# Performance work log

Hardware: AMD Instinct MI355X
Metric: run time of the kernel (lower is better)

Reference implementation:

```python
import jax, jax.numpy as jnp
import numpy as np

N = 50000        # nodes
E = 1_600_000    # edges (avg degree 32)
IN, HID, OUT = 128, 64, 16


def setup_inputs() -> dict:
    key = jax.random.key(0)
    k0, k1, k2, k3, k4 = jax.random.split(key, 5)
    src = jax.random.randint(k0, (E,), 0, N, dtype=jnp.int32)
    dst = jax.random.randint(k1, (E,), 0, N, dtype=jnp.int32)
    features = jax.random.normal(k2, (N, IN), dtype=jnp.float32)
    W1 = jax.random.normal(k3, (IN, HID), dtype=jnp.float32) / np.float32(np.sqrt(IN))
    b1 = jnp.zeros((HID,), jnp.float32)
    W2 = jax.random.normal(k4, (HID, OUT), dtype=jnp.float32) / np.float32(np.sqrt(HID))
    b2 = jnp.zeros((OUT,), jnp.float32)
    return {"features": features, "W1": W1, "b1": b1, "W2": W2, "b2": b2,
            "src": src, "dst": dst}


def _graph_conv(src, dst, x, W, b):
    # DGL GraphConv, norm='both':  out = D_dst^{-1/2} * A^T * (D_src^{-1/2} * x) @ W + b
    ones = jnp.ones((src.shape[0],), x.dtype)
    deg_out = jax.ops.segment_sum(ones, src, num_segments=N)  # out-degree of source nodes
    deg_in = jax.ops.segment_sum(ones, dst, num_segments=N)   # in-degree of dest nodes
    norm_s = jax.lax.rsqrt(jnp.maximum(deg_out, 1.0))
    norm_d = jax.lax.rsqrt(jnp.maximum(deg_in, 1.0))
    # project first (in_feats >= out_feats) so messages are in the smaller dim
    h = (x * norm_s[:, None]) @ W                              # [N, out_dim]
    agg = jax.ops.segment_sum(h[src], dst, num_segments=N)     # sparse aggregate
    return agg * norm_d[:, None] + b


def reference(features, W1, b1, W2, b2, src, dst):
    h = jax.nn.relu(_graph_conv(src, dst, features, W1, b1))
    return _graph_conv(src, dst, h, W2, b2)
```

## Files before the change

kernel.cpp:

```cpp
#include <hip/hip_runtime.h>
#include <hip/hip_fp16.h>

#define IN_F  128
#define HID_F 64
#define OUT_F 16
#define MAX_N 50176
#define HWORDS (MAX_N / 2)
#define QWORDS (MAX_N / 4)
#define NSEG  128

#define SCAN_ELEMS 4
#define SCAN_BLOCK 256
#define SCAN_CHUNK (SCAN_BLOCK * SCAN_ELEMS)

#define LSTR 136

typedef __attribute__((ext_vector_type(8))) _Float16 half8;
typedef __attribute__((ext_vector_type(4))) _Float16 half4v;
typedef __attribute__((ext_vector_type(4))) float    floatx4;

__global__ __launch_bounds__(1024) void hist2_kernel(const int* __restrict__ src,
                                                     const int* __restrict__ dst,
                                                     unsigned int* __restrict__ partial,
                                                     int E, int seg, int Wr8) {
    __shared__ unsigned int cnt[QWORDS];
    int b = blockIdx.x;
    const int* ids = blockIdx.y ? dst : src;
    unsigned int* pbase = partial + (size_t)blockIdx.y * NSEG * Wr8;
    for (int w = threadIdx.x; w < Wr8; w += 1024) cnt[w] = 0;
    __syncthreads();
    int lo = b * seg, hi = min(lo + seg, E);
    for (int e = lo + threadIdx.x; e < hi; e += 1024) {
        int d = ids[e];
        atomicAdd(&cnt[d >> 2], 1u << ((d & 3) * 8));
    }
    __syncthreads();
    for (int w = threadIdx.x; w < Wr8; w += 1024)
        pbase[(size_t)b * Wr8 + w] = cnt[w];
}

__global__ __launch_bounds__(256) void reduce_norm_kernel(unsigned int* __restrict__ partial,
                                                          int* __restrict__ counts,
                                                          float* __restrict__ norm_s,
                                                          float* __restrict__ norm_d,
                                                          int Wr8, int N) {
    int w = blockIdx.x * 256 + threadIdx.x;
    if (w >= Wr8) return;
    unsigned int r0 = 0, r1 = 0, r2 = 0, r3 = 0;
    if (blockIdx.y == 0) {
        const unsigned int* base = partial;
        for (int b = 0; b < NSEG; b++) {
            unsigned int v = base[(size_t)b * Wr8 + w];
            r0 += v & 0xFFu; r1 += (v >> 8) & 0xFFu;
            r2 += (v >> 16) & 0xFFu; r3 += v >> 24;
        }
        int d = 4 * w;
        if (d     < N) norm_s[d]     = rsqrtf(fmaxf((float)r0, 1.0f));
        if (d + 1 < N) norm_s[d + 1] = rsqrtf(fmaxf((float)r1, 1.0f));
        if (d + 2 < N) norm_s[d + 2] = rsqrtf(fmaxf((float)r2, 1.0f));
        if (d + 3 < N) norm_s[d + 3] = rsqrtf(fmaxf((float)r3, 1.0f));
    } else {
        unsigned int* base = partial + (size_t)NSEG * Wr8;
        for (int b = 0; b < NSEG; b++) {
            size_t idx = (size_t)b * Wr8 + w;
            unsigned int v = base[idx];
            base[idx] = r0 | (r1 << 8) | (r2 << 16) | (r3 << 24);
            r0 += v & 0xFFu; r1 += (v >> 8) & 0xFFu;
            r2 += (v >> 16) & 0xFFu; r3 += v >> 24;
        }
        int d = 4 * w;
        if (d     < N) { counts[d]     = (int)r0; norm_d[d]     = rsqrtf(fmaxf((float)r0, 1.0f)); }
        if (d + 1 < N) { counts[d + 1] = (int)r1; norm_d[d + 1] = rsqrtf(fmaxf((float)r1, 1.0f)); }
        if (d + 2 < N) { counts[d + 2] = (int)r2; norm_d[d + 2] = rsqrtf(fmaxf((float)r2, 1.0f)); }
        if (d + 3 < N) { counts[d + 3] = (int)r3; norm_d[d + 3] = rsqrtf(fmaxf((float)r3, 1.0f)); }
    }
}

__global__ __launch_bounds__(SCAN_BLOCK) void scan_local_kernel(int* __restrict__ counts,
                                                                int* __restrict__ bsum, int N) {
    __shared__ int part[SCAN_BLOCK];
    int t = threadIdx.x;
    int base = blockIdx.x * SCAN_CHUNK + t * SCAN_ELEMS;
    int v[SCAN_ELEMS];
    int s = 0;
    #pragma unroll
    for (int k = 0; k < SCAN_ELEMS; k++) {
        int i = base + k;
        v[k] = (i < N) ? counts[i] : 0;
        s += v[k];
    }
    part[t] = s;
    __syncthreads();
    for (int off = 1; off < SCAN_BLOCK; off <<= 1) {
        int x = (t >= off) ? part[t - off] : 0;
        __syncthreads();
        part[t] += x;
        __syncthreads();
    }
    int run = (t > 0) ? part[t - 1] : 0;
    #pragma unroll
    for (int k = 0; k < SCAN_ELEMS; k++) {
        int i = base + k;
        if (i < N) counts[i] = run;
        run += v[k];
    }
    if (t == SCAN_BLOCK - 1) bsum[blockIdx.x] = part[SCAN_BLOCK - 1];
}

__global__ __launch_bounds__(1024) void scan_bsum_kernel(int* __restrict__ bsum, int nblocks) {
    __shared__ int part[1024];
    int t = threadIdx.x;
    int v = (t < nblocks) ? bsum[t] : 0;
    part[t] = v;
    __syncthreads();
    for (int off = 1; off < 1024; off <<= 1) {
        int x = (t >= off) ? part[t - off] : 0;
        __syncthreads();
        part[t] += x;
        __syncthreads();
    }
    if (t < nblocks) bsum[t] = part[t] - v;
}

__global__ __launch_bounds__(1024) void scatter_lds_kernel(const int* __restrict__ src,
                                                           const int* __restrict__ dst,
                                                           const int* __restrict__ row_start,
                                                           const int* __restrict__ bsum,
                                                           const unsigned int* __restrict__ prefix,
                                                           unsigned short* __restrict__ csr_src,
                                                           int E, int seg, int Wr8, int N) {
    __shared__ unsigned int pos[HWORDS];
    int b = blockIdx.x;
    int p = blockIdx.y;
    int lo = b * seg, hi = min(lo + seg, E);
    int nlo = p * HWORDS, nhi = min(nlo + HWORDS, N);
    for (int d = nlo + threadIdx.x; d < nhi; d += 1024) {
        unsigned int word = prefix[(size_t)b * Wr8 + (d >> 2)];
        unsigned int base8 = (word >> ((d & 3) * 8)) & 0xFFu;
        pos[d - nlo] = (unsigned int)(row_start[d] + bsum[d >> 10]) + base8;
    }
    __syncthreads();
    for (int e = lo + threadIdx.x; e < hi; e += 1024) {
        int d = dst[e];
        if (d >= nlo && d < nhi) {
            unsigned int q = atomicAdd(&pos[d - nlo], 1u);
            csr_src[q] = (unsigned short)src[e];
        }
    }
}

__global__ __launch_bounds__(256) void gemm1_kernel(const float* __restrict__ x,
                                                    const float* __restrict__ W,
                                                    const float* __restrict__ norm_s,
                                                    __half* __restrict__ h, int N) {
    __shared__ _Float16 sx[64 * LSTR];
    __shared__ _Float16 sw[64 * LSTR];
    int t = threadIdx.x;
    int row0 = blockIdx.x * 64;

    for (int i = t; i < IN_F * 16; i += 256) {
        int k = i >> 4, n4 = (i & 15) * 4;
        float4 w4 = *(const float4*)(W + (size_t)k * HID_F + n4);
        sw[(n4 + 0) * LSTR + k] = (_Float16)w4.x;
        sw[(n4 + 1) * LSTR + k] = (_Float16)w4.y;
        sw[(n4 + 2) * LSTR + k] = (_Float16)w4.z;
        sw[(n4 + 3) * LSTR + k] = (_Float16)w4.w;
    }
    for (int i = t; i < 64 * 32; i += 256) {
        int r = i >> 5, k4 = (i & 31) * 4;
        int gr = row0 + r;
        half4v hv = {0, 0, 0, 0};
        if (gr < N) {
            float4 v = *(const float4*)(x + (size_t)gr * IN_F + k4);
            float ns = norm_s[gr];
            hv.x = (_Float16)(v.x * ns); hv.y = (_Float16)(v.y * ns);
            hv.z = (_Float16)(v.z * ns); hv.w = (_Float16)(v.w * ns);
        }
        *(half4v*)(sx + r * LSTR + k4) = hv;
    }
    __syncthreads();

    int wave = t >> 6, lane = t & 63;
    int m = lane & 15, quad = lane >> 4;
    int rbase = wave * 16;

    floatx4 acc[4] = {{0,0,0,0}, {0,0,0,0}, {0,0,0,0}, {0,0,0,0}};
    #pragma unroll
    for (int ks = 0; ks < 4; ks++) {
        half8 av = *(half8*)(sx + (rbase + m) * LSTR + ks * 32 + quad * 8);
        #pragma unroll
        for (int ct = 0; ct < 4; ct++) {
            half8 bv = *(half8*)(sw + (ct * 16 + m) * LSTR + ks * 32 + quad * 8);
            acc[ct] = __builtin_amdgcn_mfma_f32_16x16x32_f16(av, bv, acc[ct], 0, 0, 0);
        }
    }
    #pragma unroll
    for (int ct = 0; ct < 4; ct++) {
        #pragma unroll
        for (int reg = 0; reg < 4; reg++) {
            int gr = row0 + rbase + quad * 4 + reg;
            if (gr < N) h[(size_t)gr * HID_F + ct * 16 + m] = __float2half(acc[ct][reg]);
        }
    }
}

__global__ __launch_bounds__(256) void agg1_kernel(const int* __restrict__ row_start,
                                                   const int* __restrict__ bsum,
                                                   const unsigned short* __restrict__ csr_src,
                                                   const __half* __restrict__ h,
                                                   const float* __restrict__ norm_d,
                                                   const float* __restrict__ norm_s,
                                                   const float* __restrict__ b1,
                                                   const float* __restrict__ W2,
                                                   __half* __restrict__ h2, int N, int E) {
    __shared__ float sW2[HID_F * OUT_F];
    __shared__ float xrow[4][HID_F];
    int t = threadIdx.x;
    for (int i = t; i < HID_F * OUT_F; i += 256) sW2[i] = W2[i];

    int wave = t >> 6, lane = t & 63;
    int node = blockIdx.x * 4 + wave;
    bool valid = node < N;
    int slot = lane >> 3;
    int fh   = lane & 7;

    if (valid) {
        int beg = row_start[node] + bsum[node >> 10];
        int end = (node + 1 < N) ? row_start[node + 1] + bsum[(node + 1) >> 10] : E;

        float f[8] = {0.f, 0.f, 0.f, 0.f, 0.f, 0.f, 0.f, 0.f};

        #define AGG1_BODY(SIDX) {                                                  \
            const uint4* p = (const uint4*)(h + (size_t)(SIDX) * HID_F + fh * 8);  \
            uint4 u = *p;                                                          \
            __half2 q0 = *(__half2*)&u.x, q1 = *(__half2*)&u.y;                    \
            __half2 q2 = *(__half2*)&u.z, q3 = *(__half2*)&u.w;                    \
            float2 g0 = __half22float2(q0), g1 = __half22float2(q1);               \
            float2 g2 = __half22float2(q2), g3 = __half22float2(q3);               \
            f[0] += g0.x; f[1] += g0.y; f[2] += g1.x; f[3] += g1.y;                \
            f[4] += g2.x; f[5] += g2.y; f[6] += g3.x; f[7] += g3.y; }

        int i = beg + slot;
        for (; i + 24 < end; i += 32) {
            int s0 = (int)csr_src[i];
            int s1 = (int)csr_src[i + 8];
            int s2 = (int)csr_src[i + 16];
            int s3 = (int)csr_src[i + 24];
            AGG1_BODY(s0); AGG1_BODY(s1); AGG1_BODY(s2); AGG1_BODY(s3);
        }
        for (; i < end; i += 8) {
            int s = (int)csr_src[i];
            AGG1_BODY(s);
        }
        #undef AGG1_BODY

        #pragma unroll
        for (int j = 0; j < 8; j++) {
            f[j] += __shfl_xor(f[j], 8);
            f[j] += __shfl_xor(f[j], 16);
            f[j] += __shfl_xor(f[j], 32);
        }

        if (slot == 0) {
            float nd = norm_d[node], ns = norm_s[node];
            const float4 bA = *(const float4*)(b1 + fh * 8);
            const float4 bB = *(const float4*)(b1 + fh * 8 + 4);
            xrow[wave][fh * 8 + 0] = fmaxf(f[0] * nd + bA.x, 0.f) * ns;
            xrow[wave][fh * 8 + 1] = fmaxf(f[1] * nd + bA.y, 0.f) * ns;
            xrow[wave][fh * 8 + 2] = fmaxf(f[2] * nd + bA.z, 0.f) * ns;
            xrow[wave][fh * 8 + 3] = fmaxf(f[3] * nd + bA.w, 0.f) * ns;
            xrow[wave][fh * 8 + 4] = fmaxf(f[4] * nd + bB.x, 0.f) * ns;
            xrow[wave][fh * 8 + 5] = fmaxf(f[5] * nd + bB.y, 0.f) * ns;
            xrow[wave][fh * 8 + 6] = fmaxf(f[6] * nd + bB.z, 0.f) * ns;
            xrow[wave][fh * 8 + 7] = fmaxf(f[7] * nd + bB.w, 0.f) * ns;
        }
    }
    __syncthreads();
    if (valid && lane < OUT_F) {
        float acc = 0.0f;
        #pragma unroll 8
        for (int k = 0; k < HID_F; k++)
            acc += xrow[wave][k] * sW2[k * OUT_F + lane];
        h2[(size_t)node * OUT_F + lane] = __float2half(acc);
    }
}

__global__ __launch_bounds__(256) void agg2_kernel(const int* __restrict__ row_start,
                                                   const int* __restrict__ bsum,
                                                   const unsigned short* __restrict__ csr_src,
                                                   const __half* __restrict__ h2,
                                                   const float* __restrict__ norm_d,
                                                   const float* __restrict__ b2,
                                                   float* __restrict__ out, int N, int E) {
    int node = blockIdx.x * 4 + (threadIdx.x >> 6);
    if (node >= N) return;
    int lane = threadIdx.x & 63;
    int slot = lane >> 2;
    int fh   = lane & 3;
    int beg = row_start[node] + bsum[node >> 10];
    int end = (node + 1 < N) ? row_start[node + 1] + bsum[(node + 1) >> 10] : E;

    float f0 = 0.f, f1 = 0.f, f2 = 0.f, f3 = 0.f;

    #define AGG2_BODY(SIDX) {                                                  \
        const uint2* p = (const uint2*)(h2 + (size_t)(SIDX) * OUT_F + fh * 4); \
        uint2 u = *p;                                                          \
        __half2 q0 = *(__half2*)&u.x, q1 = *(__half2*)&u.y;                    \
        float2 g0 = __half22float2(q0), g1 = __half22float2(q1);               \
        f0 += g0.x; f1 += g0.y; f2 += g1.x; f3 += g1.y; }

    int i = beg + slot;
    for (; i + 16 < end; i += 32) {
        int s0 = (int)csr_src[i];
        int s1 = (int)csr_src[i + 16];
        AGG2_BODY(s0); AGG2_BODY(s1);
    }
    if (i < end) {
        int s = (int)csr_src[i];
        AGG2_BODY(s);
    }
    #undef AGG2_BODY

    f0 += __shfl_xor(f0, 4);  f1 += __shfl_xor(f1, 4);
    f2 += __shfl_xor(f2, 4);  f3 += __shfl_xor(f3, 4);
    f0 += __shfl_xor(f0, 8);  f1 += __shfl_xor(f1, 8);
    f2 += __shfl_xor(f2, 8);  f3 += __shfl_xor(f3, 8);
    f0 += __shfl_xor(f0, 16); f1 += __shfl_xor(f1, 16);
    f2 += __shfl_xor(f2, 16); f3 += __shfl_xor(f3, 16);
    f0 += __shfl_xor(f0, 32); f1 += __shfl_xor(f1, 32);
    f2 += __shfl_xor(f2, 32); f3 += __shfl_xor(f3, 32);

    if (slot == 0) {
        float nd = norm_d[node];
        float4 v;
        v.x = f0 * nd + b2[fh * 4 + 0];
        v.y = f1 * nd + b2[fh * 4 + 1];
        v.z = f2 * nd + b2[fh * 4 + 2];
        v.w = f3 * nd + b2[fh * 4 + 3];
        *(float4*)(out + (size_t)node * OUT_F + fh * 4) = v;
    }
}

extern "C" void kernel_launch(void* const* d_in, const int* in_sizes, int n_in,
                              void* d_out, int out_size, void* d_ws, size_t ws_size,
                              hipStream_t stream) {
    const float* feat = (const float*)d_in[0];
    const float* W1   = (const float*)d_in[1];
    const float* b1   = (const float*)d_in[2];
    const float* W2   = (const float*)d_in[3];
    const float* b2   = (const float*)d_in[4];
    const int*   src  = (const int*)d_in[5];
    const int*   dst  = (const int*)d_in[6];

    const int N   = in_sizes[0] / IN_F;
    const int E   = in_sizes[5];
    const int seg = (E + NSEG - 1) / NSEG;
    const int Wr8 = (N + 3) >> 2;
    const int nchunks = (N + SCAN_CHUNK - 1) / SCAN_CHUNK;
    const int npass   = (N + HWORDS - 1) / HWORDS;

    float* fws    = (float*)d_ws;
    float* norm_s = fws;
    float* norm_d = fws + N;
    __half* h1    = (__half*)(fws + 2 * (size_t)N);
    __half* h2    = h1 + (size_t)N * HID_F;
    int*   iws    = (int*)(h2 + (size_t)N * OUT_F);
    int*   row_start = iws;
    int*   bsum      = iws + N + 1;
    unsigned int* partial = (unsigned int*)(iws + N + 1 + 1024);
    unsigned short* csr_src = (unsigned short*)(partial + 2 * (size_t)NSEG * Wr8);

    hist2_kernel<<<dim3(NSEG, 2), 1024, 0, stream>>>(src, dst, partial, E, seg, Wr8);
    reduce_norm_kernel<<<dim3((Wr8 + 255) / 256, 2), 256, 0, stream>>>(partial, row_start, norm_s, norm_d, Wr8, N);

    scan_local_kernel<<<nchunks, SCAN_BLOCK, 0, stream>>>(row_start, bsum, N);
    scan_bsum_kernel<<<1, 1024, 0, stream>>>(bsum, nchunks);

    scatter_lds_kernel<<<dim3(NSEG, npass), 1024, 0, stream>>>(src, dst, row_start, bsum,
                                                               partial + (size_t)NSEG * Wr8,
                                                               csr_src, E, seg, Wr8, N);

    gemm1_kernel<<<(N + 63) / 64, 256, 0, stream>>>(feat, W1, norm_s, h1, N);
    agg1_kernel<<<(N + 3) / 4, 256, 0, stream>>>(row_start, bsum, csr_src, h1, norm_d, norm_s, b1, W2, h2, N, E);
    agg2_kernel<<<(N + 3) / 4, 256, 0, stream>>>(row_start, bsum, csr_src, h2, norm_d, b2, (float*)d_out, N, E);
}
```

Measured before the change: 212.5 us.

## Process 16 nodes per block in agg1 and use all threads for W2 projection

Each wave in agg1 now aggregates four consecutive nodes instead of one. Row-start offsets are loaded once per wave, and the W2 staging in shared memory is amortised over 16 nodes per block instead of 4. The 64x16 projection now runs across all 256 threads using a transposed, padded W2 and float4 shared-memory reads, where previously only 16 lanes per wave did the work. The cost is less block-level parallelism (about 3.1k blocks) and serial per-node latency within each wave, which may reduce how well gather latency is hidden.

```diff
diff --git a/kernel.cpp b/kernel.cpp
--- a/kernel.cpp
+++ b/kernel.cpp
@@ -14,6 +14,7 @@
 #define SCAN_CHUNK (SCAN_BLOCK * SCAN_ELEMS)
 
 #define LSTR 136
+#define XSTR 68
 
 typedef __attribute__((ext_vector_type(8))) _Float16 half8;
 typedef __attribute__((ext_vector_type(4))) _Float16 half4v;
@@ -213,75 +214,96 @@
                                                    const float* __restrict__ b1,
                                                    const float* __restrict__ W2,
                                                    __half* __restrict__ h2, int N, int E) {
-    __shared__ float sW2[HID_F * OUT_F];
-    __shared__ float xrow[4][HID_F];
+    __shared__ float sW2T[OUT_F][XSTR];
+    __shared__ float xrow[16][XSTR];
     int t = threadIdx.x;
-    for (int i = t; i < HID_F * OUT_F; i += 256) sW2[i] = W2[i];
+    for (int i = t; i < HID_F * OUT_F; i += 256) {
+        int k = i >> 4, o = i & 15;
+        sW2T[o][k] = W2[i];
+    }
 
     int wave = t >> 6, lane = t & 63;
-    int node = blockIdx.x * 4 + wave;
-    bool valid = node < N;
     int slot = lane >> 3;
     int fh   = lane & 7;
-
-    if (valid) {
-        int beg = row_start[node] + bsum[node >> 10];
-        int end = (node + 1 < N) ? row_start[node + 1] + bsum[(node + 1) >> 10] : E;
-
-        float f[8] = {0.f, 0.f, 0.f, 0.f, 0.f, 0.f, 0.f, 0.f};
-
-        #define AGG1_BODY(SIDX) {                                                  \
-            const uint4* p = (const uint4*)(h + (size_t)(SIDX) * HID_F + fh * 8);  \
-            uint4 u = *p;                                                          \
-            __half2 q0 = *(__half2*)&u.x, q1 = *(__half2*)&u.y;                    \
-            __half2 q2 = *(__half2*)&u.z, q3 = *(__half2*)&u.w;                    \
-            float2 g0 = __half22float2(q0), g1 = __half22float2(q1);               \
-            float2 g2 = __half22float2(q2), g3 = __half22float2(q3);               \
-            f[0] += g0.x; f[1] += g0.y; f[2] += g1.x; f[3] += g1.y;                \
-            f[4] += g2.x; f[5] += g2.y; f[6] += g3.x; f[7] += g3.y; }
-
-        int i = beg + slot;
-        for (; i + 24 < end; i += 32) {
-            int s0 = (int)csr_src[i];
-            int s1 = (int)csr_src[i + 8];
-            int s2 = (int)csr_src[i + 16];
-            int s3 = (int)csr_src[i + 24];
-            AGG1_BODY(s0); AGG1_BODY(s1); AGG1_BODY(s2); AGG1_BODY(s3);
-        }
-        for (; i < end; i += 8) {
-            int s = (int)csr_src[i];
-            AGG1_BODY(s);
-        }
-        #undef AGG1_BODY
-
+    int nbase = blockIdx.x * 16 + wave * 4;
+
+    int rs[5];
+    #pragma unroll
+    for (int j = 0; j < 5; j++) {
+        int n = nbase + j;
+        rs[j] = (n < N) ? (row_start[n] + bsum[n >> 10]) : E;
+    }
+
+    #pragma unroll
+    for (int nn = 0; nn < 4; nn++) {
+        int node = nbase + nn;
+        if (node < N) {
+            int beg = rs[nn], end = rs[nn + 1];
+
+            float f[8] = {0.f, 0.f, 0.f, 0.f, 0.f, 0.f, 0.f, 0.f};
+
+            #define AGG1_BODY(SIDX) {                                                  \
+                const uint4* p = (const uint4*)(h + (size_t)(SIDX) * HID_F + fh * 8);  \
+                uint4 u = *p;                                                          \
+                __half2 q0 = *(__half2*)&u.x, q1 = *(__half2*)&u.y;                    \
+                __half2 q2 = *(__half2*)&u.z, q3 = *(__half2*)&u.w;                    \
+                float2 g0 = __half22float2(q0), g1 = __half22float2(q1);               \
+                float2 g2 = __half22float2(q2), g3 = __half22float2(q3);               \
+                f[0] += g0.x; f[1] += g0.y; f[2] += g1.x; f[3] += g1.y;                \
+                f[4] += g2.x; f[5] += g2.y; f[6] += g3.x; f[7] += g3.y; }
+
+            int i = beg + slot;
+            for (; i + 24 < end; i += 32) {
+                int s0 = (int)csr_src[i];
+                int s1 = (int)csr_src[i + 8];
+                int s2 = (int)csr_src[i + 16];
+                int s3 = (int)csr_src[i + 24];
+                AGG1_BODY(s0); AGG1_BODY(s1); AGG1_BODY(s2); AGG1_BODY(s3);
+            }
+            for (; i < end; i += 8) {
+                int s = (int)csr_src[i];
+                AGG1_BODY(s);
+            }
+            #undef AGG1_BODY
+
+            #pragma unroll
+            for (int j = 0; j < 8; j++) {
+                f[j] += __shfl_xor(f[j], 8);
+                f[j] += __shfl_xor(f[j], 16);
+                f[j] += __shfl_xor(f[j], 32);
+            }
+
+            if (slot == 0) {
+                float nd = norm_d[node], ns = norm_s[node];
+                const float4 bA = *(const float4*)(b1 + fh * 8);
+                const float4 bB = *(const float4*)(b1 + fh * 8 + 4);
+                float4 vA, vB;
+                vA.x = fmaxf(f[0] * nd + bA.x, 0.f) * ns;
+                vA.y = fmaxf(f[1] * nd + bA.y, 0.f) * ns;
+                vA.z = fmaxf(f[2] * nd + bA.z, 0.f) * ns;
+                vA.w = fmaxf(f[3] * nd + bA.w, 0.f) * ns;
+                vB.x = fmaxf(f[4] * nd + bB.x, 0.f) * ns;
+                vB.y = fmaxf(f[5] * nd + bB.y, 0.f) * ns;
+                vB.z = fmaxf(f[6] * nd + bB.z, 0.f) * ns;
+                vB.w = fmaxf(f[7] * nd + bB.w, 0.f) * ns;
+                *(float4*)&xrow[wave * 4 + nn][fh * 8]     = vA;
+                *(float4*)&xrow[wave * 4 + nn][fh * 8 + 4] = vB;
+            }
+        }
+    }
+    __syncthreads();
+
+    int nr = t >> 4, o = t & 15;
+    int gnode = blockIdx.x * 16 + nr;
+    if (gnode < N) {
+        float acc = 0.0f;
         #pragma unroll
-        for (int j = 0; j < 8; j++) {
-            f[j] += __shfl_xor(f[j], 8);
-            f[j] += __shfl_xor(f[j], 16);
-            f[j] += __shfl_xor(f[j], 32);
-        }
-
-        if (slot == 0) {
-            float nd = norm_d[node], ns = norm_s[node];
-            const float4 bA = *(const float4*)(b1 + fh * 8);
-            const float4 bB = *(const float4*)(b1 + fh * 8 + 4);
-            xrow[wave][fh * 8 + 0] = fmaxf(f[0] * nd + bA.x, 0.f) * ns;
-            xrow[wave][fh * 8 + 1] = fmaxf(f[1] * nd + bA.y, 0.f) * ns;
-            xrow[wave][fh * 8 + 2] = fmaxf(f[2] * nd + bA.z, 0.f) * ns;
-            xrow[wave][fh * 8 + 3] = fmaxf(f[3] * nd + bA.w, 0.f) * ns;
-            xrow[wave][fh * 8 + 4] = fmaxf(f[4] * nd + bB.x, 0.f) * ns;
-            xrow[wave][fh * 8 + 5] = fmaxf(f[5] * nd + bB.y, 0.f) * ns;
-            xrow[wave][fh * 8 + 6] = fmaxf(f[6] * nd + bB.z, 0.f) * ns;
-            xrow[wave][fh * 8 + 7] = fmaxf(f[7] * nd + bB.w, 0.f) * ns;
-        }
-    }
-    __syncthreads();
-    if (valid && lane < OUT_F) {
-        float acc = 0.0f;
-        #pragma unroll 8
-        for (int k = 0; k < HID_F; k++)
-            acc += xrow[wave][k] * sW2[k * OUT_F + lane];
-        h2[(size_t)node * OUT_F + lane] = __float2half(acc);
+        for (int k4 = 0; k4 < HID_F / 4; k4++) {
+            float4 x4 = *(const float4*)&xrow[nr][k4 * 4];
+            float4 w4 = *(const float4*)&sW2T[o][k4 * 4];
+            acc += x4.x * w4.x + x4.y * w4.y + x4.z * w4.z + x4.w * w4.w;
+        }
+        h2[(size_t)gnode * OUT_F + o] = __float2half(acc);
     }
 }
 
@@ -381,6 +403,6 @@
                                                                csr_src, E, seg, Wr8, N);
 
     gemm1_kernel<<<(N + 63) / 64, 256, 0, stream>>>(feat, W1, norm_s, h1, N);
-    agg1_kernel<<<(N + 3) / 4, 256, 0, stream>>>(row_start, bsum, csr_src, h1, norm_d, norm_s, b1, W2, h2, N, E);
+    agg1_kernel<<<(N + 15) / 16, 256, 0, stream>>>(row_start, bsum, csr_src, h1, norm_d, norm_s, b1, W2, h2, N, E);
     agg2_kernel<<<(N + 3) / 4, 256, 0, stream>>>(row_start, bsum, csr_src, h2, norm_d, b2, (float*)d_out, N, E);
 }
```

Result: faster. 201.7 us, median of 2 (-5.1%).
